# Performance work log

Hardware: AMD Instinct MI355X
Metric: run time of the kernel (lower is better)

## Reference

```python
import jax, jax.numpy as jnp
import numpy as np
from jax import lax

D, NTOK, HEADS, DH, DEPTH, KCODE = 512, 256, 16, 32, 12, 2048

def _ln(x, g, b):
    m = x.mean(-1, keepdims=True)
    v = x.var(-1, keepdims=True)
    return (x - m) / jnp.sqrt(v + 1e-5) * g + b

def _attn(x, g, bln, wqkv, wo, bo):
    b, n, _ = x.shape
    xn = _ln(x, g, bln)
    qkv = xn @ wqkv  # [b,n,3*H*DH]
    q, k, v = jnp.split(qkv, 3, axis=-1)
    def h(t):
        return t.reshape(b, n, HEADS, DH).transpose(0, 2, 1, 3)  # bhnd
    q, k, v = h(q), h(k), h(v)
    dots = jnp.einsum('bhid,bhjd->bhij', q, k) * (DH ** -0.5)
    a = jax.nn.softmax(dots, axis=-1)
    o = jnp.einsum('bhij,bhjd->bhid', a, v).transpose(0, 2, 1, 3).reshape(b, n, HEADS * DH)
    return x + o @ wo + bo

def _conv3(x, w):  # w [out,in,3,3], pad 1
    return lax.conv_general_dilated(x, w, (1, 1), [(1, 1), (1, 1)],
                                    dimension_numbers=('NCHW', 'OIHW', 'NCHW'))

def _convT2(x, w, b):  # torch ConvTranspose2d k=2,s=2; w torch-shape [in,out,2,2]
    wk = jnp.transpose(w, (1, 0, 2, 3))[:, :, ::-1, ::-1]
    y = lax.conv_general_dilated(x, wk, (1, 1), [(1, 1), (1, 1)], lhs_dilation=(2, 2),
                                 dimension_numbers=('NCHW', 'OIHW', 'NCHW'))
    return y + b[None, :, None, None]

def _bn_relu(x, g, b):  # training-mode BatchNorm2d (biased var) + ReLU
    m = x.mean((0, 2, 3), keepdims=True)
    v = x.var((0, 2, 3), keepdims=True)
    xn = (x - m) / jnp.sqrt(v + 1e-5)
    return jax.nn.relu(xn * g[None, :, None, None] + b[None, :, None, None])

def setup_inputs() -> dict:
    key = jax.random.key(0)
    ks = iter(jax.random.split(key, 64))
    r = lambda *s: jax.random.normal(next(ks), s, dtype=jnp.float32)
    w = lambda *s: 0.02 * jax.random.normal(next(ks), s, dtype=jnp.float32)
    inp = {
        'x': r(16, 512, 16, 16),
        'feat0': r(16, 64, 128, 128),
        'feat1': r(16, 128, 64, 64),
        'feat2': r(16, 256, 32, 32),
        'pos_emb': r(1, NTOK, D),
        'codebook': r(KCODE, D),
        'ln_g': jnp.ones((DEPTH, D)), 'ln_b': jnp.zeros((DEPTH, D)),
        'wqkv': w(DEPTH, D, 3 * HEADS * DH),
        'wo': w(DEPTH, HEADS * DH, D), 'bo': jnp.zeros((DEPTH, D)),
        'up_w0': w(512, 256, 2, 2), 'up_b0': jnp.zeros((256,)),
        'cw0a': w(256, 512, 3, 3), 'g0a': jnp.ones((256,)), 'b0a': jnp.zeros((256,)),
        'cw0b': w(256, 256, 3, 3), 'g0b': jnp.ones((256,)), 'b0b': jnp.zeros((256,)),
        'up_w1': w(256, 128, 2, 2), 'up_b1': jnp.zeros((128,)),
        'cw1a': w(128, 256, 3, 3), 'g1a': jnp.ones((128,)), 'b1a': jnp.zeros((128,)),
        'cw1b': w(128, 128, 3, 3), 'g1b': jnp.ones((128,)), 'b1b': jnp.zeros((128,)),
        'up_w2': w(128, 64, 2, 2), 'up_b2': jnp.zeros((64,)),
        'cw2a': w(64, 128, 3, 3), 'g2a': jnp.ones((64,)), 'b2a': jnp.zeros((64,)),
        'cw2b': w(64, 64, 3, 3), 'g2b': jnp.ones((64,)), 'b2b': jnp.zeros((64,)),
        'last_w': w(1, 64, 1, 1), 'last_b': jnp.zeros((1,)),
    }
    return inp

def reference(x, feat0, feat1, feat2, pos_emb, codebook, ln_g, ln_b, wqkv, wo, bo,
              up_w0, up_b0, cw0a, g0a, b0a, cw0b, g0b, b0b,
              up_w1, up_b1, cw1a, g1a, b1a, cw1b, g1b, b1b,
              up_w2, up_b2, cw2a, g2a, b2a, cw2b, g2b, b2b,
              last_w, last_b):
    b = x.shape[0]
    # ViT encoder: flatten spatial -> tokens, add pos embedding, 12 residual attn layers
    tok = x.reshape(b, D, NTOK).transpose(0, 2, 1) + pos_emb  # [b,256,512]
    for i in range(DEPTH):
        tok = _attn(tok, ln_g[i], ln_b[i], wqkv[i], wo[i], bo[i])
    # VQ codebook quantization: squared-euclidean argmin + gather + straight-through
    flat = tok.reshape(-1, D)
    d2 = (flat * flat).sum(-1, keepdims=True) - 2.0 * flat @ codebook.T + (codebook * codebook).sum(-1)
    idx = jnp.argmin(d2, axis=-1)
    q = codebook[idx].reshape(b, NTOK, D)
    quant = tok + lax.stop_gradient(q - tok)
    y = quant.transpose(0, 2, 1).reshape(b, D, 16, 16)
    # conv decoder with skip connections (DecoderCup blocks)
    y = _convT2(y, up_w0, up_b0)                      # [b,256,32,32]
    y = jnp.concatenate([y, feat2], axis=1)           # [b,512,32,32]
    y = _bn_relu(_conv3(y, cw0a), g0a, b0a)
    y = _bn_relu(_conv3(y, cw0b), g0b, b0b)
    y = _convT2(y, up_w1, up_b1)                      # [b,128,64,64]
    y = jnp.concatenate([y, feat1], axis=1)
    y = _bn_relu(_conv3(y, cw1a), g1a, b1a)
    y = _bn_relu(_conv3(y, cw1b), g1b, b1b)
    y = _convT2(y, up_w2, up_b2)                      # [b,64,128,128]
    y = jnp.concatenate([y, feat0], axis=1)
    y = _bn_relu(_conv3(y, cw2a), g2a, b2a)
    y = _bn_relu(_conv3(y, cw2b), g2b, b2b)
    y = lax.conv_general_dilated(y, last_w, (1, 1), [(0, 0), (0, 0)],
                                 dimension_numbers=('NCHW', 'OIHW', 'NCHW')) + last_b[None, :, None, None]
    return jax.nn.sigmoid(y)  # [b,1,128,128]
```

## Files before the change

kernel.cpp:

```cpp
#include <hip/hip_runtime.h>

#define B_    16
#define NTOK  256
#define D_    512
#define HEADS 16
#define DH    32
#define DEPTH 12
#define KCODE 2048
#define M_    (B_*NTOK)
#define BN_S  512

typedef __attribute__((ext_vector_type(8))) short short8;
typedef __attribute__((ext_vector_type(4))) float float4v;
typedef __attribute__((ext_vector_type(4))) unsigned int uint4v;
typedef __attribute__((ext_vector_type(2))) unsigned int uint2v;
typedef unsigned short ushort;

__device__ __forceinline__ ushort f2b(float f){
  union { float f; unsigned u; } v; v.f = f;
  unsigned r = v.u + 0x7FFFu + ((v.u >> 16) & 1u);
  return (ushort)(r >> 16);
}
__device__ __forceinline__ float b2f(ushort h){
  union { unsigned u; float f; } v; v.u = ((unsigned)h) << 16; return v.f;
}
__device__ __forceinline__ float bits2f(unsigned u){
  union { unsigned u; float f; } v; v.u = u; return v.f;
}

typedef __attribute__((address_space(3))) unsigned int lds_uint;
typedef __attribute__((address_space(1))) const unsigned int glob_uint;
__device__ __forceinline__ void gl_lds16(const ushort* g, ushort* l){
  __builtin_amdgcn_global_load_lds((glob_uint*)g, (lds_uint*)l, 16, 0, 0);
}


__global__ void k_tok_init(const float* __restrict__ x, const float* __restrict__ pos,
                           float* __restrict__ tok){
  __shared__ float t[32][33];
  const int t0 = blockIdx.x*32, d0 = blockIdx.y*32, b = blockIdx.z;
  const int tx = threadIdx.x, ty = threadIdx.y;
  #pragma unroll
  for (int i = 0; i < 4; ++i){
    int d = d0 + ty + i*8;
    t[ty + i*8][tx] = x[((size_t)(b*D_ + d))*NTOK + t0 + tx];
  }
  __syncthreads();
  #pragma unroll
  for (int i = 0; i < 4; ++i){
    int tt = t0 + ty + i*8;
    tok[((size_t)(b*NTOK + tt))*D_ + d0 + tx] = t[tx][ty + i*8] + pos[(size_t)tt*D_ + d0 + tx];
  }
}

__global__ void k_split(const float* __restrict__ src, ushort* __restrict__ oh,
                        ushort* __restrict__ ol, int n){
  int i = blockIdx.x*256 + threadIdx.x;
  if (i >= n) return;
  float v = src[i];
  ushort h = f2b(v);
  oh[i] = h; ol[i] = f2b(v - b2f(h));
}

__global__ void k_split_t(const float* __restrict__ src, ushort* __restrict__ oh,
                          ushort* __restrict__ ol, int K, int N){
  __shared__ float t[32][33];
  const int n0 = blockIdx.x*32, k0 = blockIdx.y*32;
  const size_t lb = (size_t)blockIdx.z*K*N;
  const int tx = threadIdx.x, ty = threadIdx.y;
  #pragma unroll
  for (int i = 0; i < 4; ++i){
    int k = k0 + ty + i*8;
    t[ty + i*8][tx] = src[lb + (size_t)k*N + n0 + tx];
  }
  __syncthreads();
  #pragma unroll
  for (int i = 0; i < 4; ++i){
    int n = n0 + ty + i*8;
    float v = t[tx][ty + i*8];
    ushort h = f2b(v);
    size_t o = lb + (size_t)n*K + k0 + tx;
    oh[o] = h; ol[o] = f2b(v - b2f(h));
  }
}

__global__ void k_w9(const float* __restrict__ w, ushort* __restrict__ W9,
                     int Cin, int Cout){
  int i = blockIdx.x*256 + threadIdx.x;
  if (i >= Cout*Cin*9) return;
  int co = i / (Cin*9); int r = i - co*(Cin*9);
  int ci = r / 9; int tap = r - ci*9;
  W9[((size_t)tap*Cout + co)*Cin + ci] = f2b(w[i]);
}

__global__ void k_upw(const float* __restrict__ w, ushort* __restrict__ Wt4,
                      int Cin, int Cout){
  int i = blockIdx.x*256 + threadIdx.x;
  if (i >= Cin*Cout*4) return;
  int ci = i / (Cout*4); int r = i - ci*(Cout*4);
  int co = r >> 2; int tap = r & 3;
  Wt4[((size_t)tap*Cout + co)*Cin + ci] = f2b(w[i]);
}

__global__ void k_ln_split(const float* __restrict__ in, ushort* __restrict__ oh,
                           ushort* __restrict__ ol, const float* __restrict__ g,
                           const float* __restrict__ bta){
  int row = blockIdx.x; int t = threadIdx.x;
  const float* xr = in + (size_t)row*D_;
  float x0 = xr[t], x1 = xr[t+256];
  __shared__ float r1[256], r2[256];
  r1[t] = x0+x1; r2[t] = x0*x0 + x1*x1;
  __syncthreads();
  for (int off=128; off>0; off>>=1){
    if (t<off){ r1[t]+=r1[t+off]; r2[t]+=r2[t+off]; }
    __syncthreads();
  }
  float mean = r1[0] * (1.f/D_);
  float var  = r2[0] * (1.f/D_) - mean*mean;
  float inv  = rsqrtf(var + 1e-5f);
  float y0 = (x0-mean)*inv*g[t]     + bta[t];
  float y1 = (x1-mean)*inv*g[t+256] + bta[t+256];
  size_t o = (size_t)row*D_;
  ushort h0 = f2b(y0), h1 = f2b(y1);
  oh[o+t] = h0;     ol[o+t]     = f2b(y0 - b2f(h0));
  oh[o+t+256] = h1; ol[o+t+256] = f2b(y1 - b2f(h1));
}

__global__ __launch_bounds__(256,2) void k_gemm_split(
    const ushort* __restrict__ Ah, const ushort* __restrict__ Al,
    const ushort* __restrict__ Bh, const ushort* __restrict__ Bl,
    float* __restrict__ C, const float* __restrict__ bias,
    const float* __restrict__ resid, int M, int N, int K){
  __shared__ ushort Ash[128][32], Asl[128][32], Bsh[128][32], Bsl[128][32];
  const int tid = threadIdx.x;
  const int m_base = blockIdx.x*128, n_base = blockIdx.y*128;
  const int lane = tid & 63, wv = tid >> 6;
  const int quad = lane >> 4, r16 = lane & 15;
  const int m_off = (wv & 1)*64, n_off = (wv >> 1)*64;
  const int lrow = lane >> 2, lseg = lane & 3;
  const int row0 = wv*32 + lrow;
  const int us   = lseg ^ ((row0 >> 1) & 3);
  const size_t offA0 = (size_t)(m_base + row0)*K + us*8;
  const size_t offA1 = offA0 + (size_t)16*K;
  const size_t offB0 = (size_t)(n_base + row0)*K + us*8;
  const size_t offB1 = offB0 + (size_t)16*K;
  ushort* lAh = &Ash[0][0] + wv*1024;
  ushort* lAl = &Asl[0][0] + wv*1024;
  ushort* lBh = &Bsh[0][0] + wv*1024;
  ushort* lBl = &Bsl[0][0] + wv*1024;
  float4v acc[4][4];
  #pragma unroll
  for (int i = 0; i < 4; ++i)
    #pragma unroll
    for (int j = 0; j < 4; ++j) acc[i][j] = float4v{0.f,0.f,0.f,0.f};
  for (int k0 = 0; k0 < K; k0 += 32){
    gl_lds16(Ah + offA0 + k0, lAh);
    gl_lds16(Ah + offA1 + k0, lAh + 512);
    gl_lds16(Al + offA0 + k0, lAl);
    gl_lds16(Al + offA1 + k0, lAl + 512);
    gl_lds16(Bh + offB0 + k0, lBh);
    gl_lds16(Bh + offB1 + k0, lBh + 512);
    gl_lds16(Bl + offB0 + k0, lBl);
    gl_lds16(Bl + offB1 + k0, lBl + 512);
    __syncthreads();
    short8 ah[4], al[4], bh[4], bl[4];
    #pragma unroll
    for (int i = 0; i < 4; ++i){
      int ra = m_off + i*16 + r16;
      int rb = n_off + i*16 + r16;
      int sa = (quad ^ ((ra >> 1) & 3))*8;
      int sb = (quad ^ ((rb >> 1) & 3))*8;
      ah[i] = *(const short8*)&Ash[ra][sa];
      al[i] = *(const short8*)&Asl[ra][sa];
      bh[i] = *(const short8*)&Bsh[rb][sb];
      bl[i] = *(const short8*)&Bsl[rb][sb];
    }
    #pragma unroll
    for (int i = 0; i < 4; ++i)
      #pragma unroll
      for (int j = 0; j < 4; ++j){
        acc[i][j] = __builtin_amdgcn_mfma_f32_16x16x32_bf16(bh[j], ah[i], acc[i][j], 0,0,0);
        acc[i][j] = __builtin_amdgcn_mfma_f32_16x16x32_bf16(bh[j], al[i], acc[i][j], 0,0,0);
        acc[i][j] = __builtin_amdgcn_mfma_f32_16x16x32_bf16(bl[j], ah[i], acc[i][j], 0,0,0);
      }
    __syncthreads();
  }
  #pragma unroll
  for (int i = 0; i < 4; ++i){
    int m = m_base + m_off + i*16 + r16;
    #pragma unroll
    for (int j = 0; j < 4; ++j){
      int n = n_base + n_off + j*16 + quad*4;
      float4v v = acc[i][j];
      if (bias)  v += *(const float4v*)(bias + n);
      if (resid) v += *(const float4v*)(resid + (size_t)m*N + n);
      *(float4v*)(C + (size_t)m*N + n) = v;
    }
  }
}

__global__ __launch_bounds__(512) void k_attn2(const float* __restrict__ qkv,
                                               ushort* __restrict__ oh,
                                               ushort* __restrict__ ol){
  __shared__ float4v smem[NTOK*16];
  float4v* ks = smem;
  float4v* vs = smem + NTOK*8;
  const int h = blockIdx.x, b = blockIdx.y, t = threadIdx.x;
  const int tq = t & 255, half = t >> 8;
  const float* base = qkv + (size_t)b*NTOK*1536;
  const int koff = 512 + h*DH, voff = 1024 + h*DH;
  for (int i = t; i < NTOK*8; i += 512){
    int j = i >> 3, d4 = i & 7;
    ks[i] = *(const float4v*)(base + (size_t)j*1536 + koff + d4*4);
    vs[i] = *(const float4v*)(base + (size_t)j*1536 + voff + d4*4);
  }
  float4v q8[8];
  const float* qrow = base + (size_t)tq*1536 + h*DH;
  #pragma unroll
  for (int d4 = 0; d4 < 8; ++d4) q8[d4] = *(const float4v*)(qrow + d4*4);
  __syncthreads();
  float4v o8[8];
  #pragma unroll
  for (int d4 = 0; d4 < 8; ++d4) o8[d4] = float4v{0.f,0.f,0.f,0.f};
  float l = 0.f;
  const int j0 = half*128, j1 = j0 + 128;
  for (int j = j0; j < j1; ++j){
    float s = 0.f;
    #pragma unroll
    for (int d4 = 0; d4 < 8; ++d4){
      float4v kk = ks[j*8 + d4];
      s += q8[d4].x*kk.x + q8[d4].y*kk.y + q8[d4].z*kk.z + q8[d4].w*kk.w;
    }
    float e = __expf(s * 0.17677669529663689f);
    l += e;
    #pragma unroll
    for (int d4 = 0; d4 < 8; ++d4){
      float4v vv = vs[j*8 + d4];
      o8[d4].x += e*vv.x; o8[d4].y += e*vv.y; o8[d4].z += e*vv.z; o8[d4].w += e*vv.w;
    }
  }
  __syncthreads();
  if (half){
    float4v* st = smem + (size_t)tq*9;
    #pragma unroll
    for (int d4 = 0; d4 < 8; ++d4) st[d4] = o8[d4];
    ((float*)smem)[9216 + tq] = l;
  }
  __syncthreads();
  if (!half){
    const float4v* st = smem + (size_t)tq*9;
    #pragma unroll
    for (int d4 = 0; d4 < 8; ++d4) o8[d4] += st[d4];
    l += ((float*)smem)[9216 + tq];
    float inv = 1.f / l;
    size_t ob = (size_t)(b*NTOK + tq)*D_ + h*DH;
    #pragma unroll
    for (int d4 = 0; d4 < 8; ++d4){
      float vals[4] = {o8[d4].x*inv, o8[d4].y*inv, o8[d4].z*inv, o8[d4].w*inv};
      #pragma unroll
      for (int r = 0; r < 4; ++r){
        ushort hh = f2b(vals[r]);
        oh[ob + d4*4 + r] = hh;
        ol[ob + d4*4 + r] = f2b(vals[r] - b2f(hh));
      }
    }
  }
}

__global__ void k_cnorm(const float* __restrict__ cb, float* __restrict__ cnorm){
  int k = blockIdx.x, t = threadIdx.x;
  float v1 = cb[(size_t)k*D_ + t];
  float v2 = cb[(size_t)k*D_ + t + 256];
  __shared__ float r[256];
  r[t] = v1*v1 + v2*v2;
  __syncthreads();
  for (int off=128; off>0; off>>=1){
    if (t<off) r[t]+=r[t+off];
    __syncthreads();
  }
  if (t==0) cnorm[k] = r[0];
}

__global__ void k_argmin(const float* __restrict__ d2, const float* __restrict__ cnorm,
                         int* __restrict__ idx){
  int m = blockIdx.x, t = threadIdx.x;
  float best = 3.4e38f; int bk = 0;
  for (int k = t; k < KCODE; k += 256){
    float s = cnorm[k] - 2.f*d2[(size_t)m*KCODE + k];
    if (s < best){ best = s; bk = k; }
  }
  __shared__ float bs[256]; __shared__ int bi[256];
  bs[t]=best; bi[t]=bk;
  __syncthreads();
  for (int off=128; off>0; off>>=1){
    if (t<off){
      if (bs[t+off] < bs[t] || (bs[t+off]==bs[t] && bi[t+off]<bi[t])){
        bs[t]=bs[t+off]; bi[t]=bi[t+off];
      }
    }
    __syncthreads();
  }
  if (t==0) idx[m] = bi[0];
}

__global__ void k_gather_nhwc(const float* __restrict__ cb, const int* __restrict__ idx,
                              ushort* __restrict__ y0){
  int i = blockIdx.x*256 + threadIdx.x;
  if (i >= B_*NTOK*D_) return;
  int d = i % D_; int r = i / D_; int t = r % NTOK; int b = r / NTOK;
  y0[i] = f2b(cb[(size_t)idx[b*NTOK + t]*D_ + d]);
}


__global__ __launch_bounds__(256) void k_conv_nhwc(
    const ushort* __restrict__ X, const ushort* __restrict__ W9,
    float* __restrict__ Y, int Cin, int Cout, int H, int W){
  __shared__ ushort Xs[128][36];
  __shared__ ushort Ws[576][36];
  const int HW = H*W;
  const int tid = threadIdx.x;
  const int b = blockIdx.z;
  const int tiles_w = W >> 3;
  const int th0 = (blockIdx.x / tiles_w) * 8;
  const int tw0 = (blockIdx.x - (blockIdx.x / tiles_w)*tiles_w) * 8;
  const int n_base = blockIdx.y*64;
  const int lane = tid & 63, wv = tid >> 6;
  const int quad = lane >> 4, r16 = lane & 15;
  const int m_off = (wv & 1)*32, n_off = (wv >> 1)*32;
  const ushort* Xb = X + (size_t)b*HW*Cin;
  const ushort* sptr[2]; int srw[2], ssg[2]; bool sok[2];
  #pragma unroll
  for (int e = 0; e < 2; ++e){
    int item = tid + e*256;
    int row = (item >> 2) & 127;
    int seg = item & 3;
    int ph = row / 10, pw = row - ph*10;
    int gh = th0 + ph - 1, gw = tw0 + pw - 1;
    bool ok = (item < 400) && gh >= 0 && gh < H && gw >= 0 && gw < W;
    int pidx = ok ? (gh*W + gw) : 0;
    srw[e] = row; ssg[e] = seg; sok[e] = ok;
    sptr[e] = Xb + ((size_t)pidx*Cin + seg*8);
  }
  const ushort* wptr[9]; int wrw[9], wsg[9];
  #pragma unroll
  for (int e = 0; e < 9; ++e){
    int item = tid + e*256;
    int row = item >> 2;
    int seg = item & 3;
    int tap = row >> 6, co = row & 63;
    wrw[e] = row; wsg[e] = seg;
    wptr[e] = W9 + ((size_t)tap*Cout + n_base + co)*Cin + seg*8;
  }
  const uint4v zz = {};
  float4v a00={}, a01={}, a10={}, a11={};
  const int mA = m_off + r16, mB = mA + 16;
  const int rA0 = ((mA>>3))*10 + (mA&7);
  const int rB0 = ((mB>>3))*10 + (mB&7);
  for (int k0 = 0; k0 < Cin; k0 += 32){
    if (k0) __syncthreads();
    #pragma unroll
    for (int e = 0; e < 2; ++e){
      uint4v v = sok[e] ? *(const uint4v*)(sptr[e] + k0) : zz;
      *(uint4v*)&Xs[srw[e]][ssg[e]*8] = v;
    }
    #pragma unroll
    for (int e = 0; e < 9; ++e)
      *(uint4v*)&Ws[wrw[e]][wsg[e]*8] = *(const uint4v*)(wptr[e] + k0);
    __syncthreads();
    #pragma unroll
    for (int tap = 0; tap < 9; ++tap){
      const int kh = tap/3, kw = tap - (tap/3)*3;
      short8 wf0 = *(const short8*)&Ws[tap*64 + n_off      + r16][quad*8];
      short8 wf1 = *(const short8*)&Ws[tap*64 + n_off + 16 + r16][quad*8];
      short8 xf0 = *(const short8*)&Xs[rA0 + kh*10 + kw][quad*8];
      short8 xf1 = *(const short8*)&Xs[rB0 + kh*10 + kw][quad*8];
      a00 = __builtin_amdgcn_mfma_f32_16x16x32_bf16(wf0, xf0, a00, 0,0,0);
      a01 = __builtin_amdgcn_mfma_f32_16x16x32_bf16(wf0, xf1, a01, 0,0,0);
      a10 = __builtin_amdgcn_mfma_f32_16x16x32_bf16(wf1, xf0, a10, 0,0,0);
      a11 = __builtin_amdgcn_mfma_f32_16x16x32_bf16(wf1, xf1, a11, 0,0,0);
    }
  }
  float* Yb = Y + (size_t)b*HW*Cout;
  int pA = (th0 + (mA>>3))*W + tw0 + (mA&7);
  int pB = (th0 + (mB>>3))*W + tw0 + (mB&7);
  int co0 = n_base + n_off + quad*4, co1 = co0 + 16;
  *(float4v*)(Yb + (size_t)pA*Cout + co0) = a00;
  *(float4v*)(Yb + (size_t)pB*Cout + co0) = a01;
  *(float4v*)(Yb + (size_t)pA*Cout + co1) = a10;
  *(float4v*)(Yb + (size_t)pB*Cout + co1) = a11;
}

__global__ __launch_bounds__(256) void k_upconv_nhwc(
    const ushort* __restrict__ X, const ushort* __restrict__ Wt4,
    const float* __restrict__ bias, ushort* __restrict__ CC,
    int Cin, int Cout, int Hi, int Wi, int Ctot){
  __shared__ ushort Xs[64][40], Ws[4][64][40];
  const int HWi = Hi*Wi;
  const int tid = threadIdx.x;
  const int b = blockIdx.z;
  const int m_base = blockIdx.x*64;
  const int n_base = blockIdx.y*64;
  const int lane = tid & 63, wv = tid >> 6;
  const int quad = lane >> 4, r16 = lane & 15;
  const int m_off = (wv & 1)*32, n_off = (wv >> 1)*32;
  const int srow = tid & 63, skq = tid >> 6;
  const ushort* xrow = X + ((size_t)b*HWi + m_base + srow)*Cin + skq*8;
  const ushort* w0 = Wt4 + ((size_t)0*Cout + n_base + srow)*Cin + skq*8;
  const ushort* w1 = Wt4 + ((size_t)1*Cout + n_base + srow)*Cin + skq*8;
  const ushort* w2 = Wt4 + ((size_t)2*Cout + n_base + srow)*Cin + skq*8;
  const ushort* w3 = Wt4 + ((size_t)3*Cout + n_base + srow)*Cin + skq*8;
  float4v acc[4][4];
  #pragma unroll
  for (int t = 0; t < 4; ++t)
    #pragma unroll
    for (int q = 0; q < 4; ++q) acc[t][q] = float4v{0.f,0.f,0.f,0.f};
  for (int k0 = 0; k0 < Cin; k0 += 32){
    *(uint4v*)&Xs[srow][skq*8]    = *(const uint4v*)(xrow + k0);
    *(uint4v*)&Ws[0][srow][skq*8] = *(const uint4v*)(w0 + k0);
    *(uint4v*)&Ws[1][srow][skq*8] = *(const uint4v*)(w1 + k0);
    *(uint4v*)&Ws[2][srow][skq*8] = *(const uint4v*)(w2 + k0);
    *(uint4v*)&Ws[3][srow][skq*8] = *(const uint4v*)(w3 + k0);
    __syncthreads();
    short8 xf0 = *(const short8*)&Xs[m_off      + r16][quad*8];
    short8 xf1 = *(const short8*)&Xs[m_off + 16 + r16][quad*8];
    #pragma unroll
    for (int t = 0; t < 4; ++t){
      short8 wf0 = *(const short8*)&Ws[t][n_off      + r16][quad*8];
      short8 wf1 = *(const short8*)&Ws[t][n_off + 16 + r16][quad*8];
      acc[t][0] = __builtin_amdgcn_mfma_f32_16x16x32_bf16(wf0, xf0, acc[t][0], 0,0,0);
      acc[t][1] = __builtin_amdgcn_mfma_f32_16x16x32_bf16(wf0, xf1, acc[t][1], 0,0,0);
      acc[t][2] = __builtin_amdgcn_mfma_f32_16x16x32_bf16(wf1, xf0, acc[t][2], 0,0,0);
      acc[t][3] = __builtin_amdgcn_mfma_f32_16x16x32_bf16(wf1, xf1, acc[t][3], 0,0,0);
    }
    __syncthreads();
  }
  const int Wo = 2*Wi, HWo = 4*HWi;
  int co0 = n_base + n_off + quad*4, co1 = co0 + 16;
  float4v bv0 = *(const float4v*)(bias + co0);
  float4v bv1 = *(const float4v*)(bias + co1);
  int px0 = m_base + m_off + r16, px1 = px0 + 16;
  #pragma unroll
  for (int j = 0; j < 2; ++j){
    int p = j ? px1 : px0;
    int r = p / Wi, c = p - r*Wi;
    #pragma unroll
    for (int t = 0; t < 4; ++t){
      int opix = (2*r + (t>>1))*Wo + 2*c + (t&1);
      ushort* o = CC + ((size_t)b*HWo + opix)*Ctot;
      float4v vA = acc[t][0 + j] + bv0;
      float4v vB = acc[t][2 + j] + bv1;
      uint2v pA, pB;
      pA.x = (unsigned)f2b(vA.x) | ((unsigned)f2b(vA.y) << 16);
      pA.y = (unsigned)f2b(vA.z) | ((unsigned)f2b(vA.w) << 16);
      pB.x = (unsigned)f2b(vB.x) | ((unsigned)f2b(vB.y) << 16);
      pB.y = (unsigned)f2b(vB.z) | ((unsigned)f2b(vB.w) << 16);
      *(uint2v*)(o + co0) = pA;
      *(uint2v*)(o + co1) = pB;
    }
  }
}

__global__ void k_feat2cc(const float* __restrict__ feat, ushort* __restrict__ cc,
                          int Cf, int Coff, int Ctot, int HW){
  __shared__ ushort t[32][33];
  int pb = blockIdx.x*32, cbs = blockIdx.y*32, b = blockIdx.z;
  int tx = threadIdx.x, ty = threadIdx.y;
  #pragma unroll
  for (int i = 0; i < 4; ++i){
    int c = cbs + ty + i*8;
    t[ty + i*8][tx] = f2b(feat[((size_t)(b*Cf) + c)*HW + pb + tx]);
  }
  __syncthreads();
  #pragma unroll
  for (int i = 0; i < 4; ++i){
    int p = pb + ty + i*8;
    cc[((size_t)b*HW + p)*Ctot + Coff + cbs + tx] = t[tx][ty + i*8];
  }
}

__global__ __launch_bounds__(256) void k_bnstats_nhwc(
    const float* __restrict__ x, float* __restrict__ part, int C, int HW){
  const int s = blockIdx.x, tid = threadIdx.x;
  const int R = B_*HW;
  const int chunk = R / BN_S;
  const int L = C >> 2;
  const int G = 256 / L;
  const int c4 = tid % L, g = tid / L;
  float4v a = {}, q = {};
  const float* xb = x + (size_t)(s*chunk)*C + 4*c4;
  for (int r = g; r < chunk; r += G){
    float4v v = *(const float4v*)(xb + (size_t)r*C);
    a += v; q += v*v;
  }
  __shared__ float4v h1[256], h2[256];
  h1[tid] = a; h2[tid] = q;
  __syncthreads();
  if (tid < L){
    float4v ra = h1[tid], rq = h2[tid];
    for (int gg = 1; gg < G; ++gg){ ra += h1[tid + gg*L]; rq += h2[tid + gg*L]; }
    int c0 = 4*c4;
    part[(size_t)(c0+0)*BN_S + s] = ra.x;
    part[(size_t)(c0+1)*BN_S + s] = ra.y;
    part[(size_t)(c0+2)*BN_S + s] = ra.z;
    part[(size_t)(c0+3)*BN_S + s] = ra.w;
    part[(size_t)(C+c0+0)*BN_S + s] = rq.x;
    part[(size_t)(C+c0+1)*BN_S + s] = rq.y;
    part[(size_t)(C+c0+2)*BN_S + s] = rq.z;
    part[(size_t)(C+c0+3)*BN_S + s] = rq.w;
  }
}

__global__ void k_bnfinal(const float* __restrict__ part, const float* __restrict__ g,
                          const float* __restrict__ bb, float* __restrict__ scale,
                          float* __restrict__ shift, int C, int cnt){
  int c = blockIdx.x, t = threadIdx.x;
  __shared__ float r1[256], r2[256];
  r1[t] = part[(size_t)c*BN_S + t]       + part[(size_t)c*BN_S + t + 256];
  r2[t] = part[(size_t)(C + c)*BN_S + t] + part[(size_t)(C + c)*BN_S + t + 256];
  __syncthreads();
  for (int off = 128; off > 0; off >>= 1){
    if (t < off){ r1[t] += r1[t+off]; r2[t] += r2[t+off]; }
    __syncthreads();
  }
  if (t == 0){
    float m = r1[0]/cnt;
    float v = r2[0]/cnt - m*m;
    float sc = g[c]*rsqrtf(v + 1e-5f);
    scale[c] = sc;
    shift[c] = bb[c] - m*sc;
  }
}

__global__ void k_bnapply_nhwc(const float* __restrict__ x, ushort* __restrict__ y,
                               const float* __restrict__ scale,
                               const float* __restrict__ shift, int C, int n4){
  int i = blockIdx.x*256 + threadIdx.x;
  if (i >= n4) return;
  float4v v = *(const float4v*)(x + (size_t)4*i);
  int c0 = (4*i) % C;
  float4v sc = *(const float4v*)(scale + c0);
  float4v sh = *(const float4v*)(shift + c0);
  float r0 = fmaxf(v.x*sc.x + sh.x, 0.f);
  float r1 = fmaxf(v.y*sc.y + sh.y, 0.f);
  float r2 = fmaxf(v.z*sc.z + sh.z, 0.f);
  float r3 = fmaxf(v.w*sc.w + sh.w, 0.f);
  uint2v pk;
  pk.x = (unsigned)f2b(r0) | ((unsigned)f2b(r1) << 16);
  pk.y = (unsigned)f2b(r2) | ((unsigned)f2b(r3) << 16);
  *(uint2v*)(y + (size_t)4*i) = pk;
}

__global__ void k_last_nhwc(const ushort* __restrict__ x, const float* __restrict__ lw,
                            const float* __restrict__ lb, float* __restrict__ out){
  __shared__ float wsm[64];
  int tid = threadIdx.x;
  if (tid < 64) wsm[tid] = lw[tid];
  __syncthreads();
  int i = blockIdx.x*256 + tid;
  const uint4v* xr = (const uint4v*)(x + (size_t)i*64);
  float acc = lb[0];
  #pragma unroll
  for (int q = 0; q < 8; ++q){
    uint4v u = xr[q];
    unsigned uu[4] = {u.x, u.y, u.z, u.w};
    #pragma unroll
    for (int k = 0; k < 4; ++k){
      acc += bits2f(uu[k] << 16)          * wsm[q*8 + 2*k];
      acc += bits2f(uu[k] & 0xffff0000u)  * wsm[q*8 + 2*k + 1];
    }
  }
  out[i] = 1.f/(1.f + __expf(-acc));
}

#define MBx 1048576ull

static inline void run_conv(const ushort* in, const float* w, ushort* W9,
                            float* out, int Cin, int Cout, int H, int W,
                            hipStream_t stream){
  int total = Cout*Cin*9;
  k_w9<<<(total+255)/256, 256, 0, stream>>>(w, W9, Cin, Cout);
  k_conv_nhwc<<<dim3((H>>3)*(W>>3), Cout/64, B_), 256, 0, stream>>>(in, W9, out, Cin, Cout, H, W);
}

static inline void run_bn(const float* x, ushort* y, float* part, float* scale, float* shift,
                          const float* g, const float* bb, int C, int HW, hipStream_t stream){
  k_bnstats_nhwc<<<BN_S, 256, 0, stream>>>(x, part, C, HW);
  k_bnfinal<<<C, 256, 0, stream>>>(part, g, bb, scale, shift, C, B_*HW);
  int n4 = B_*HW*C/4;
  k_bnapply_nhwc<<<(n4+255)/256, 256, 0, stream>>>(x, y, scale, shift, C, n4);
}

extern "C" void kernel_launch(void* const* d_in, const int* in_sizes, int n_in,
                              void* d_out, int out_size, void* d_ws, size_t ws_size,
                              hipStream_t stream){
  const float* x     = (const float*)d_in[0];
  const float* feat0 = (const float*)d_in[1];
  const float* feat1 = (const float*)d_in[2];
  const float* feat2 = (const float*)d_in[3];
  const float* pos   = (const float*)d_in[4];
  const float* cb    = (const float*)d_in[5];
  const float* ln_g  = (const float*)d_in[6];
  const float* ln_b  = (const float*)d_in[7];
  const float* wqkv  = (const float*)d_in[8];
  const float* wo    = (const float*)d_in[9];
  const float* bo    = (const float*)d_in[10];
  const float* up_w0 = (const float*)d_in[11];
  const float* up_b0 = (const float*)d_in[12];
  const float* cw0a  = (const float*)d_in[13];
  const float* g0a   = (const float*)d_in[14];
  const float* b0a   = (const float*)d_in[15];
  const float* cw0b  = (const float*)d_in[16];
  const float* g0b   = (const float*)d_in[17];
  const float* b0b   = (const float*)d_in[18];
  const float* up_w1 = (const float*)d_in[19];
  const float* up_b1 = (const float*)d_in[20];
  const float* cw1a  = (const float*)d_in[21];
  const float* g1a   = (const float*)d_in[22];
  const float* b1a   = (const float*)d_in[23];
  const float* cw1b  = (const float*)d_in[24];
  const float* g1b   = (const float*)d_in[25];
  const float* b1b   = (const float*)d_in[26];
  const float* up_w2 = (const float*)d_in[27];
  const float* up_b2 = (const float*)d_in[28];
  const float* cw2a  = (const float*)d_in[29];
  const float* g2a   = (const float*)d_in[30];
  const float* b2a   = (const float*)d_in[31];
  const float* cw2b  = (const float*)d_in[32];
  const float* g2b   = (const float*)d_in[33];
  const float* b2b   = (const float*)d_in[34];
  const float* lw    = (const float*)d_in[35];
  const float* lb    = (const float*)d_in[36];

  char* ws = (char*)d_ws;
  float*  tok     = (float*) (ws);
  ushort* xn_hi   = (ushort*)(ws +  8388608ull);
  ushort* xn_lo   = (ushort*)(ws + 12582912ull);
  float*  qkv     = (float*) (ws + 16777216ull);
  ushort* at_hi   = (ushort*)(ws + 41943040ull);
  ushort* at_lo   = (ushort*)(ws + 46137344ull);
  ushort* tok_hi  = (ushort*)(ws + 50331648ull);
  ushort* tok_lo  = (ushort*)(ws + 54525952ull);
  ushort* Wq_hi   = (ushort*)(ws + 58720256ull);
  ushort* Wq_lo   = (ushort*)(ws + 77594624ull);
  ushort* Wo_hi   = (ushort*)(ws + 96468992ull);
  ushort* Wo_lo   = (ushort*)(ws + 102760448ull);
  ushort* cb_hi   = (ushort*)(ws + 109051904ull);
  ushort* cb_lo   = (ushort*)(ws + 111149056ull);
  float*  cnorm   = (float*) (ws + 113246208ull);
  int*    idx     = (int*)   (ws + 113254400ull);
  float*  d2      = (float*) (ws + 58720256ull);
  ushort* W9   = (ushort*)(ws + 134*MBx);
  float* bnsc  = (float*) (ws + 136*MBx + 524288);
  float* bnsh  = (float*) (ws + 136*MBx + 528384);
  ushort* Wt4  = (ushort*)(ws + 137*MBx);
  float* bnp   = (float*) (ws + 138*MBx);
  ushort* y0   = (ushort*)(ws + 139*MBx);
  ushort* cc0 = (ushort*)(ws + 146*MBx);
  float*  va0 = (float*) (ws + 163*MBx);
  ushort* xa0 = (ushort*)(ws + 180*MBx);
  float*  vb0 = (float*) (ws + 146*MBx);
  ushort* xb0 = (ushort*)(ws + 189*MBx);
  ushort* cc1 = (ushort*)(ws + 0*MBx);
  float*  va1 = (float*) (ws + 34*MBx);
  ushort* xa1 = (ushort*)(ws + 68*MBx);
  float*  vb1 = (float*) (ws + 85*MBx);
  ushort* xb1 = (ushort*)(ws + 146*MBx);
  ushort* cc2 = (ushort*)(ws + 0*MBx);
  float*  va2 = (float*) (ws + 67*MBx);
  ushort* xa2 = (ushort*)(ws + 146*MBx);
  float*  vb2 = (float*) (ws + 0*MBx);
  ushort* xb2 = (ushort*)(ws + 67*MBx);

  k_split_t<<<dim3(1536/32, D_/32, DEPTH), dim3(32,8), 0, stream>>>(wqkv, Wq_hi, Wq_lo, D_, 1536);
  k_split_t<<<dim3(D_/32, D_/32, DEPTH), dim3(32,8), 0, stream>>>(wo, Wo_hi, Wo_lo, D_, D_);
  k_split<<<(KCODE*D_+255)/256, 256, 0, stream>>>(cb, cb_hi, cb_lo, KCODE*D_);
  k_cnorm<<<KCODE, 256, 0, stream>>>(cb, cnorm);

  k_tok_init<<<dim3(NTOK/32, D_/32, B_), dim3(32,8), 0, stream>>>(x, pos, tok);
  for (int l = 0; l < DEPTH; ++l){
    k_ln_split<<<M_, 256, 0, stream>>>(tok, xn_hi, xn_lo, ln_g + l*D_, ln_b + l*D_);
    k_gemm_split<<<dim3(M_/128, 1536/128), 256, 0, stream>>>(
        xn_hi, xn_lo, Wq_hi + (size_t)l*1536*D_, Wq_lo + (size_t)l*1536*D_,
        qkv, nullptr, nullptr, M_, 1536, D_);
    k_attn2<<<dim3(HEADS, B_), 512, 0, stream>>>(qkv, at_hi, at_lo);
    k_gemm_split<<<dim3(M_/128, D_/128), 256, 0, stream>>>(
        at_hi, at_lo, Wo_hi + (size_t)l*D_*D_, Wo_lo + (size_t)l*D_*D_,
        tok, bo + l*D_, tok, M_, D_, D_);
  }

  k_split<<<(M_*D_+255)/256, 256, 0, stream>>>(tok, tok_hi, tok_lo, M_*D_);
  k_gemm_split<<<dim3(M_/128, KCODE/128), 256, 0, stream>>>(
      tok_hi, tok_lo, cb_hi, cb_lo, d2, nullptr, nullptr, M_, KCODE, D_);
  k_argmin<<<M_, 256, 0, stream>>>(d2, cnorm, idx);
  k_gather_nhwc<<<(B_*NTOK*D_)/256, 256, 0, stream>>>(cb, idx, y0);

  k_upw<<<(512*256*4+255)/256, 256, 0, stream>>>(up_w0, Wt4, 512, 256);
  k_upconv_nhwc<<<dim3(256/64, 256/64, B_), 256, 0, stream>>>(y0, Wt4, up_b0, cc0, 512, 256, 16, 16, 512);
  k_feat2cc<<<dim3(1024/32, 256/32, B_), dim3(32,8), 0, stream>>>(feat2, cc0, 256, 256, 512, 1024);
  run_conv(cc0, cw0a, W9, va0, 512, 256, 32, 32, stream);
  run_bn(va0, xa0, bnp, bnsc, bnsh, g0a, b0a, 256, 1024, stream);
  run_conv(xa0, cw0b, W9, vb0, 256, 256, 32, 32, stream);
  run_bn(vb0, xb0, bnp, bnsc, bnsh, g0b, b0b, 256, 1024, stream);

  k_upw<<<(256*128*4+255)/256, 256, 0, stream>>>(up_w1, Wt4, 256, 128);
  k_upconv_nhwc<<<dim3(1024/64, 128/64, B_), 256, 0, stream>>>(xb0, Wt4, up_b1, cc1, 256, 128, 32, 32, 256);
  k_feat2cc<<<dim3(4096/32, 128/32, B_), dim3(32,8), 0, stream>>>(feat1, cc1, 128, 128, 256, 4096);
  run_conv(cc1, cw1a, W9, va1, 256, 128, 64, 64, stream);
  run_bn(va1, xa1, bnp, bnsc, bnsh, g1a, b1a, 128, 4096, stream);
  run_conv(xa1, cw1b, W9, vb1, 128, 128, 64, 64, stream);
  run_bn(vb1, xb1, bnp, bnsc, bnsh, g1b, b1b, 128, 4096, stream);

  k_upw<<<(128*64*4+255)/256, 256, 0, stream>>>(up_w2, Wt4, 128, 64);
  k_upconv_nhwc<<<dim3(4096/64, 64/64, B_), 256, 0, stream>>>(xb1, Wt4, up_b2, cc2, 128, 64, 64, 64, 128);
  k_feat2cc<<<dim3(16384/32, 64/32, B_), dim3(32,8), 0, stream>>>(feat0, cc2, 64, 64, 128, 16384);
  run_conv(cc2, cw2a, W9, va2, 128, 64, 128, 128, stream);
  run_bn(va2, xa2, bnp, bnsc, bnsh, g2a, b2a, 64, 16384, stream);
  run_conv(xa2, cw2b, W9, vb2, 64, 64, 128, 128, stream);
  run_bn(vb2, xb2, bnp, bnsc, bnsh, g2b, b2b, 64, 16384, stream);

  k_last_nhwc<<<(B_*16384)/256, 256, 0, stream>>>(xb2, lw, lb, (float*)d_out);
}
```

Before: 2.235 ms.

## Add 16x16 spatial-tile conv kernel using 32x32 MFMA for large decoder convs

Adds a new implicit-GEMM 3x3 conv kernel that tiles 16x16 output pixels (an 18x18 halo) by 64 output channels and uses 32x32x16 bf16 MFMA instructions with 64x64 per-wave accumulators. It replaces the 8x8-tile kernel for the four convs at 64x64 and 128x128 resolution. The larger tile cuts halo overhead and reloading of weights and inputs per output, and the larger MFMA shape raises arithmetic per LDS read. In exchange it uses more LDS and registers, lowering occupancy, and it has no double buffering.

Result: faster. 2.187 ms (-2.1%).

```diff
diff --git a/kernel.cpp b/kernel.cpp
--- a/kernel.cpp
+++ b/kernel.cpp
@@ -12,6 +12,7 @@
 
 typedef __attribute__((ext_vector_type(8))) short short8;
 typedef __attribute__((ext_vector_type(4))) float float4v;
+typedef __attribute__((ext_vector_type(16))) float float16v;
 typedef __attribute__((ext_vector_type(4))) unsigned int uint4v;
 typedef __attribute__((ext_vector_type(2))) unsigned int uint2v;
 typedef unsigned short ushort;
@@ -390,6 +391,100 @@
   *(float4v*)(Yb + (size_t)pB*Cout + co1) = a11;
 }
 
+__global__ __launch_bounds__(256,2) void k_conv16(
+    const ushort* __restrict__ X, const ushort* __restrict__ W9,
+    float* __restrict__ Y, int Cin, int Cout, int H, int W){
+  __shared__ ushort Xs[324][34];
+  __shared__ ushort Ws[576][34];
+  const int HW = H*W;
+  const int tid = threadIdx.x;
+  const int b = blockIdx.z;
+  const int tiles_w = W >> 4;
+  const int th0 = (blockIdx.x / tiles_w) * 16;
+  const int tw0 = (blockIdx.x - (blockIdx.x / tiles_w)*tiles_w) * 16;
+  const int n_base = blockIdx.y*64;
+  const int lane = tid & 63, wv = tid >> 6;
+  const int l31 = lane & 31, hi8 = (lane >> 5)*8;
+  const ushort* Xb = X + (size_t)b*HW*Cin;
+  const ushort* sptr[6]; ushort* sdst[6]; bool sok[6];
+  #pragma unroll
+  for (int e = 0; e < 6; ++e){
+    int item = tid + e*256;
+    int row = item >> 2;
+    int seg = item & 3;
+    if (row > 323) row = 323;
+    int ph = row / 18, pw = row - ph*18;
+    int gh = th0 + ph - 1, gw = tw0 + pw - 1;
+    bool ok = gh >= 0 && gh < H && gw >= 0 && gw < W;
+    int pidx = ok ? (gh*W + gw) : 0;
+    sok[e] = ok;
+    sptr[e] = Xb + ((size_t)pidx*Cin + seg*8);
+    sdst[e] = &Xs[row][seg*8];
+  }
+  const ushort* wptr[9]; ushort* wdst[9];
+  #pragma unroll
+  for (int e = 0; e < 9; ++e){
+    int item = tid + e*256;
+    int row = item >> 2;
+    int seg = item & 3;
+    int tap = row >> 6, co = row & 63;
+    wdst[e] = &Ws[row][seg*8];
+    wptr[e] = W9 + ((size_t)tap*Cout + n_base + co)*Cin + seg*8;
+  }
+  const uint4v zz = {};
+  float16v a00={}, a01={}, a10={}, a11={};
+  const int lrow = (lane & 15) + ((lane & 16) ? 18 : 0);
+  const int pr0 = wv*72 + lrow;
+  for (int k0 = 0; k0 < Cin; k0 += 32){
+    if (k0) __syncthreads();
+    #pragma unroll
+    for (int e = 0; e < 6; ++e){
+      if (e < 5 || tid < 16){
+        uint4v v = sok[e] ? *(const uint4v*)(sptr[e] + k0) : zz;
+        *(uint4v*)sdst[e] = v;
+      }
+    }
+    #pragma unroll
+    for (int e = 0; e < 9; ++e)
+      *(uint4v*)wdst[e] = *(const uint4v*)(wptr[e] + k0);
+    __syncthreads();
+    #pragma unroll
+    for (int s = 0; s < 2; ++s){
+      const int kc = s*16 + hi8;
+      #pragma unroll
+      for (int tap = 0; tap < 9; ++tap){
+        const int kh = tap/3, kw = tap - (tap/3)*3;
+        const int xr = pr0 + kh*18 + kw;
+        short8 x0 = *(const short8*)&Xs[xr     ][kc];
+        short8 x1 = *(const short8*)&Xs[xr + 36][kc];
+        short8 w0 = *(const short8*)&Ws[tap*64      + l31][kc];
+        short8 w1 = *(const short8*)&Ws[tap*64 + 32 + l31][kc];
+        a00 = __builtin_amdgcn_mfma_f32_32x32x16_bf16(w0, x0, a00, 0,0,0);
+        a01 = __builtin_amdgcn_mfma_f32_32x32x16_bf16(w0, x1, a01, 0,0,0);
+        a10 = __builtin_amdgcn_mfma_f32_32x32x16_bf16(w1, x0, a10, 0,0,0);
+        a11 = __builtin_amdgcn_mfma_f32_32x32x16_bf16(w1, x1, a11, 0,0,0);
+      }
+    }
+  }
+  float* Yb = Y + (size_t)b*HW*Cout;
+  const int co4 = (lane >> 5)*4;
+  #pragma unroll
+  for (int i = 0; i < 2; ++i){
+    int p = wv*64 + i*32 + l31;
+    int gp = (th0 + (p >> 4))*W + tw0 + (p & 15);
+    float* yr = Yb + (size_t)gp*Cout + n_base + co4;
+    float16v A0 = i ? a01 : a00;
+    float16v A1 = i ? a11 : a10;
+    #pragma unroll
+    for (int q = 0; q < 4; ++q){
+      float4v v0 = {A0[4*q+0], A0[4*q+1], A0[4*q+2], A0[4*q+3]};
+      float4v v1 = {A1[4*q+0], A1[4*q+1], A1[4*q+2], A1[4*q+3]};
+      *(float4v*)(yr + 8*q)      = v0;
+      *(float4v*)(yr + 32 + 8*q) = v1;
+    }
+  }
+}
+
 __global__ __launch_bounds__(256) void k_upconv_nhwc(
     const ushort* __restrict__ X, const ushort* __restrict__ Wt4,
     const float* __restrict__ bias, ushort* __restrict__ CC,
@@ -580,6 +675,14 @@
   int total = Cout*Cin*9;
   k_w9<<<(total+255)/256, 256, 0, stream>>>(w, W9, Cin, Cout);
   k_conv_nhwc<<<dim3((H>>3)*(W>>3), Cout/64, B_), 256, 0, stream>>>(in, W9, out, Cin, Cout, H, W);
+}
+
+static inline void run_conv16(const ushort* in, const float* w, ushort* W9,
+                              float* out, int Cin, int Cout, int H, int W,
+                              hipStream_t stream){
+  int total = Cout*Cin*9;
+  k_w9<<<(total+255)/256, 256, 0, stream>>>(w, W9, Cin, Cout);
+  k_conv16<<<dim3((H>>4)*(W>>4), Cout/64, B_), 256, 0, stream>>>(in, W9, out, Cin, Cout, H, W);
 }
 
 static inline void run_bn(const float* x, ushort* y, float* part, float* scale, float* shift,
@@ -705,17 +808,17 @@
   k_upw<<<(256*128*4+255)/256, 256, 0, stream>>>(up_w1, Wt4, 256, 128);
   k_upconv_nhwc<<<dim3(1024/64, 128/64, B_), 256, 0, stream>>>(xb0, Wt4, up_b1, cc1, 256, 128, 32, 32, 256);
   k_feat2cc<<<dim3(4096/32, 128/32, B_), dim3(32,8), 0, stream>>>(feat1, cc1, 128, 128, 256, 4096);
-  run_conv(cc1, cw1a, W9, va1, 256, 128, 64, 64, stream);
+  run_conv16(cc1, cw1a, W9, va1, 256, 128, 64, 64, stream);
   run_bn(va1, xa1, bnp, bnsc, bnsh, g1a, b1a, 128, 4096, stream);
-  run_conv(xa1, cw1b, W9, vb1, 128, 128, 64, 64, stream);
+  run_conv16(xa1, cw1b, W9, vb1, 128, 128, 64, 64, stream);
   run_bn(vb1, xb1, bnp, bnsc, bnsh, g1b, b1b, 128, 4096, stream);
 
   k_upw<<<(128*64*4+255)/256, 256, 0, stream>>>(up_w2, Wt4, 128, 64);
   k_upconv_nhwc<<<dim3(4096/64, 64/64, B_), 256, 0, stream>>>(xb1, Wt4, up_b2, cc2, 128, 64, 64, 64, 128);
   k_feat2cc<<<dim3(16384/32, 64/32, B_), dim3(32,8), 0, stream>>>(feat0, cc2, 64, 64, 128, 16384);
-  run_conv(cc2, cw2a, W9, va2, 128, 64, 128, 128, stream);
+  run_conv16(cc2, cw2a, W9, va2, 128, 64, 128, 128, stream);
   run_bn(va2, xa2, bnp, bnsc, bnsh, g2a, b2a, 64, 16384, stream);
-  run_conv(xa2, cw2b, W9, vb2, 64, 64, 128, 128, stream);
+  run_conv16(xa2, cw2b, W9, vb2, 64, 64, 128, 128, stream);
   run_bn(vb2, xb2, bnp, bnsc, bnsh, g2b, b2b, 64, 16384, stream);
 
   k_last_nhwc<<<(B_*16384)/256, 256, 0, stream>>>(xb2, lw, lb, (float*)d_out);
```
